# Kernel optimization log

Measured on AMD Instinct MI355X. Metric: run time of the kernel, lower is better.

Reference implementation:

```python
import jax, jax.numpy as jnp
import numpy as np

D = 1024
H = 16
HD = D // H
DS = 64
B, L = 2, 2048


def setup_inputs() -> dict:
    key = jax.random.key(0)
    ks = jax.random.split(key, 12)
    s = 0.02
    return {
        "x": jax.random.normal(ks[0], (B, L, D), jnp.float32),
        "subject_embed": jax.random.normal(ks[1], (B, DS), jnp.float32),
        "key_padding_mask": jnp.zeros((B, L), jnp.bool_),
        "Wq": jax.random.normal(ks[2], (D, D), jnp.float32) * s,
        "Wk": jax.random.normal(ks[3], (D, D), jnp.float32) * s,
        "Wv": jax.random.normal(ks[4], (D, D), jnp.float32) * s,
        "Wo": jax.random.normal(ks[5], (D, D), jnp.float32) * s,
        "bo": jnp.zeros((D,), jnp.float32),
        "Wsq": jax.random.normal(ks[6], (DS, D), jnp.float32) * s,
        "bsq": jnp.zeros((D,), jnp.float32),
        "Wsk": jax.random.normal(ks[7], (DS, D), jnp.float32) * s,
        "bsk": jnp.zeros((D,), jnp.float32),
    }


def reference(x, subject_embed, key_padding_mask, Wq, Wk, Wv, Wo, bo, Wsq, bsq, Wsk, bsk):
    scale = 1.0 / jnp.sqrt(jnp.asarray(HD, x.dtype))
    q = x @ Wq + (subject_embed @ Wsq + bsq)[:, None, :]   # [B,L,D]
    k = x @ Wk + (subject_embed @ Wsk + bsk)[:, None, :]
    v = x @ Wv
    # split heads: [B,H,L,hd]
    q = q.reshape(B, L, H, HD).transpose(0, 2, 1, 3)
    k = k.reshape(B, L, H, HD).transpose(0, 2, 1, 3)
    v = v.reshape(B, L, H, HD).transpose(0, 2, 1, 3)
    attn = jnp.einsum('bhqd,bhkd->bhqk', q, k) * scale      # [B,H,L,L]
    attn = jnp.where(key_padding_mask[:, None, None, :], -jnp.inf, attn)
    attn = jax.nn.softmax(attn, axis=-1)
    out = jnp.einsum('bhqk,bhkd->bhqd', attn, v)
    out = out.transpose(0, 2, 1, 3).reshape(B, L, D)
    return out @ Wo + bo
```

## Files before the change

### kernel.cpp

```cpp
#include <hip/hip_runtime.h>
#include <hip/hip_bf16.h>
#include <math.h>

#define DEV __device__ __forceinline__

typedef short bf16x8 __attribute__((ext_vector_type(8)));
typedef short bf16x4 __attribute__((ext_vector_type(4)));
typedef float f32x4 __attribute__((ext_vector_type(4)));

static constexpr int D  = 1024;
static constexpr int H  = 16;
static constexpr int HD = 64;
static constexpr int DS = 64;
static constexpr int B  = 2;
static constexpr int L  = 2048;
static constexpr int M  = B * L;

static constexpr float QSCALE = 0.18033688011112042f;

DEV unsigned short f2bf(float f) {
  union { float f; unsigned u; } x; x.f = f;
  unsigned r = (x.u + 0x7FFFu + ((x.u >> 16) & 1u)) >> 16;
  return (unsigned short)r;
}

DEV unsigned pack2bf(float a, float b) {
  return (unsigned)f2bf(a) | ((unsigned)f2bf(b) << 16);
}

DEV unsigned pack2bf_trunc(float a, float b) {
  union { float f; unsigned u; } ua{a}, ub{b};
  return (ua.u >> 16) | (ub.u & 0xffff0000u);
}

DEV void gload_lds16(const void* g, void* l) {
  __builtin_amdgcn_global_load_lds(
      (const __attribute__((address_space(1))) unsigned int*)g,
      (__attribute__((address_space(3))) unsigned int*)l, 16, 0, 0);
}

__global__ __launch_bounds__(256) void prep_kernel(
    const float* __restrict__ Wq, const float* __restrict__ Wk,
    const float* __restrict__ Wv, const float* __restrict__ Wo,
    const float* __restrict__ x, const float* __restrict__ subj,
    const float* __restrict__ Wsq, const float* __restrict__ bsq,
    const float* __restrict__ Wsk, const float* __restrict__ bsk,
    unsigned short* __restrict__ WT4, unsigned short* __restrict__ xb,
    float* __restrict__ sq, float* __restrict__ sk) {
  __shared__ float tile[64][65];
  const int blk = blockIdx.x, t = threadIdx.x;
  if (blk < 1024) {
    const int z = blk >> 8, idx = blk & 255;
    const float* W = z == 0 ? Wq : z == 1 ? Wk : z == 2 ? Wv : Wo;
    unsigned short* dst = WT4 + (size_t)z * D * D;
    const int n0 = (idx & 15) * 64, k0 = (idx >> 4) * 64;
    const int c = t & 63, r4 = t >> 6;
#pragma unroll
    for (int rr = 0; rr < 16; ++rr) {
      int row = r4 + rr * 4;
      tile[row][c] = W[(size_t)(k0 + row) * D + n0 + c];
    }
    __syncthreads();
#pragma unroll
    for (int rr = 0; rr < 16; ++rr) {
      int nrow = r4 + rr * 4;
      dst[(size_t)(n0 + nrow) * D + k0 + c] = f2bf(tile[c][nrow]);
    }
  } else if (blk < 3072) {
    size_t g = (size_t)(blk - 1024) * 256 + t;
    const float4* xf = (const float4*)x;
    float4 a = xf[2 * g], b = xf[2 * g + 1];
    union { unsigned short s[8]; uint4 v; } o;
    o.s[0] = f2bf(a.x); o.s[1] = f2bf(a.y); o.s[2] = f2bf(a.z); o.s[3] = f2bf(a.w);
    o.s[4] = f2bf(b.x); o.s[5] = f2bf(b.y); o.s[6] = f2bf(b.z); o.s[7] = f2bf(b.w);
    ((uint4*)xb)[g] = o.v;
  } else {
    int g = (blk - 3072) * 256 + t;
    int ty = g >> 11, b = (g >> 10) & 1, n = g & 1023;
    const float* W = ty ? Wsk : Wsq;
    const float* bias = ty ? bsk : bsq;
    float s = bias[n];
#pragma unroll 8
    for (int d = 0; d < DS; ++d) s += subj[b * DS + d] * W[d * D + n];
    (ty ? sk : sq)[b * D + n] = s;
  }
}

__global__ __launch_bounds__(256) void proj_kernel(
    const unsigned short* __restrict__ xb, const unsigned short* __restrict__ WT3,
    const float* __restrict__ sq, const float* __restrict__ sk,
    unsigned short* __restrict__ qk, unsigned short* __restrict__ vT) {
  __shared__ __align__(16) unsigned short smem[128 * 136];
  unsigned short* As = smem;
  unsigned short* Bs = smem + 128 * 64;
  const int z = blockIdx.z;
  const unsigned short* Wt = WT3 + (size_t)z * D * D;
  const int m0 = blockIdx.y * 128, n0 = blockIdx.x * 128;
  const int t = threadIdx.x, l = t & 63, w = t >> 6;
  const int wm = w >> 1, wn = w & 1;
  const int lm = l & 15, lq = l >> 4;
  const int srow8 = t >> 3;
  const int fsw = ((t & 7) ^ ((t >> 3) & 7)) * 8;
  const int swm = lm & 7;
  f32x4 acc[4][4] = {};
  for (int kt = 0; kt < D / 64; ++kt) {
    const int kb = kt * 64;
#pragma unroll
    for (int c = 0; c < 4; ++c) {
      int row = 32 * c + srow8;
      gload_lds16(&xb[(size_t)(m0 + row) * D + kb + fsw], &As[(32 * c + 8 * w) * 64]);
      gload_lds16(&Wt[(size_t)(n0 + row) * D + kb + fsw], &Bs[(32 * c + 8 * w) * 64]);
    }
    __syncthreads();
#pragma unroll
    for (int kk = 0; kk < 2; ++kk) {
      bf16x8 af[4], bf[4];
#pragma unroll
      for (int i = 0; i < 4; ++i)
        af[i] = *(const bf16x8*)&As[(64 * wm + 16 * i + lm) * 64 + ((kk * 4 + lq) ^ swm) * 8];
#pragma unroll
      for (int j = 0; j < 4; ++j)
        bf[j] = *(const bf16x8*)&Bs[(64 * wn + 16 * j + lm) * 64 + ((kk * 4 + lq) ^ swm) * 8];
#pragma unroll
      for (int i = 0; i < 4; ++i)
#pragma unroll
        for (int j = 0; j < 4; ++j)
          acc[i][j] = __builtin_amdgcn_mfma_f32_16x16x32_bf16(af[i], bf[j], acc[i][j], 0, 0, 0);
    }
    __syncthreads();
  }
  if (z == 2) {
#pragma unroll
    for (int i = 0; i < 4; ++i)
#pragma unroll
      for (int j = 0; j < 4; ++j) {
        int cr = 64 * wn + 16 * j + lm;
        int rr = 64 * wm + 16 * i + 4 * lq;
        uint2 u;
        u.x = pack2bf(acc[i][j][0], acc[i][j][1]);
        u.y = pack2bf(acc[i][j][2], acc[i][j][3]);
        *(uint2*)&smem[cr * 136 + rr] = u;
      }
    __syncthreads();
    const int cr = t >> 1, half = t & 1;
    const int bb = m0 >> 11, l0 = m0 & (L - 1);
    const int gcol = n0 + cr, h = gcol >> 6, hd = gcol & 63;
    size_t dbase = ((size_t)(bb * H + h) * HD + hd) * L + l0 + half * 64;
#pragma unroll
    for (int c = 0; c < 8; ++c) {
      uint4 u = *(const uint4*)&smem[cr * 136 + half * 64 + c * 8];
      *(uint4*)&vT[dbase + c * 8] = u;
    }
  } else {
    unsigned short* dst = qk + (size_t)z * M * D;
    const float* bias = z == 0 ? sq : sk;
    const float post = z == 0 ? QSCALE : 1.0f;
#pragma unroll
    for (int i = 0; i < 4; ++i)
#pragma unroll
      for (int j = 0; j < 4; ++j)
#pragma unroll
        for (int r = 0; r < 4; ++r) {
          int rr = 64 * wm + 16 * i + 4 * lq + r;
          int cc = 64 * wn + 16 * j + lm;
          float v = (acc[i][j][r] + bias[((m0 + rr) >> 11) * D + n0 + cc]) * post;
          smem[rr * 136 + cc] = f2bf(v);
        }
    __syncthreads();
    const int row = t >> 1, half = t & 1;
    const int bb = m0 >> 11, ll = (m0 & (L - 1)) + row;
    const int h0 = (n0 >> 6) + half;
    size_t dbase = ((size_t)(bb * H + h0) * L + ll) * HD;
#pragma unroll
    for (int c = 0; c < 8; ++c) {
      uint4 u = *(const uint4*)&smem[row * 136 + half * 64 + c * 8];
      *(uint4*)&dst[dbase + c * 8] = u;
    }
  }
}

__global__ __launch_bounds__(512, 4) void attn_kernel(
    const unsigned short* __restrict__ q_hm, const unsigned short* __restrict__ k_hm,
    const unsigned short* __restrict__ vT, const unsigned char* __restrict__ mask,
    unsigned short* __restrict__ ctx) {
  __shared__ __align__(16) unsigned short smem[40960];
  unsigned short* Qs  = smem;
  unsigned short* Ksb = smem + 8192;
  unsigned short* Vtb = smem + 24576;
  const int bx = blockIdx.x;
  const int rest = bx >> 3;
  const int bhid = (bx & 7) + 8 * (rest >> 4);
  const int q0 = (rest & 15) * 128;
  const int h = bhid & 15, b = bhid >> 4;
  const size_t bh = (size_t)(b * H + h);
  const unsigned short* qp = q_hm + bh * L * HD;
  const unsigned short* kp = k_hm + bh * L * HD;
  const unsigned short* vp = vT + bh * HD * L;
  const int t = threadIdx.x, l = t & 63, w = t >> 6;
  const int wq = w & 3, wj = w >> 2;
  const int lm = l & 15, lq = l >> 4;
  const int fsw = ((t & 7) ^ ((t >> 3) & 7)) * 8;
  const int swm = lm & 7;
  const int srow = t >> 3;
  const int vs = t & 15, vr = t >> 4;
  const int vcsrc = ((vs & 8) | ((vs & 7) ^ (vr & 7))) * 8;

#pragma unroll
  for (int c = 0; c < 2; ++c) {
    gload_lds16(&qp[(size_t)(q0 + 64 * c + srow) * HD + fsw], &Qs[(64 * c + 8 * w) * 64]);
    gload_lds16(&kp[(size_t)(64 * c + srow) * HD + fsw], &Ksb[(64 * c + 8 * w) * 64]);
    gload_lds16(&vp[(size_t)(32 * c + vr) * L + vcsrc], &Vtb[(32 * c + 4 * w) * 128]);
  }
  __syncthreads();
  bf16x8 qf[2][2];
#pragma unroll
  for (int i = 0; i < 2; ++i)
#pragma unroll
    for (int kk = 0; kk < 2; ++kk)
      qf[i][kk] = *(const bf16x8*)&Qs[(wq * 32 + 16 * i + lm) * 64 + ((kk * 4 + lq) ^ swm) * 8];

  float lsum[2] = {0.f, 0.f};
  f32x4 ot[2][4] = {};

  for (int kt = 0; kt < L / 128; ++kt) {
    const int cur = kt & 1;
    const unsigned short* Kc = Ksb + cur * 8192;
    const unsigned short* Vc = Vtb + cur * 8192;
    unsigned char mby = mask[b * L + kt * 128 + 64 * wj + l];
    if (kt + 1 < L / 128) {
      const int nk0 = (kt + 1) * 128;
      unsigned short* Kd = Ksb + (cur ^ 1) * 8192;
      unsigned short* Vd = Vtb + (cur ^ 1) * 8192;
#pragma unroll
      for (int c = 0; c < 2; ++c) {
        gload_lds16(&kp[(size_t)(nk0 + 64 * c + srow) * HD + fsw], &Kd[(64 * c + 8 * w) * 64]);
        gload_lds16(&vp[(size_t)(32 * c + vr) * L + nk0 + vcsrc], &Vd[(32 * c + 4 * w) * 128]);
      }
    }
    unsigned long long mb = __ballot(mby != 0);

#pragma unroll
    for (int jt4 = 0; jt4 < 4; ++jt4) {
      const int jt = 4 * wj + jt4;
      bf16x8 kf0 = *(const bf16x8*)&Kc[(16 * jt + lm) * 64 + ((0 + lq) ^ swm) * 8];
      bf16x8 kf1 = *(const bf16x8*)&Kc[(16 * jt + lm) * 64 + ((4 + lq) ^ swm) * 8];
      f32x4 st[2];
#pragma unroll
      for (int i = 0; i < 2; ++i) {
        f32x4 a = {};
        a = __builtin_amdgcn_mfma_f32_16x16x32_bf16(kf0, qf[i][0], a, 0, 0, 0);
        a = __builtin_amdgcn_mfma_f32_16x16x32_bf16(kf1, qf[i][1], a, 0, 0, 0);
        st[i] = a;
      }
      if (mb) {
        unsigned bits = (unsigned)(mb >> (4 * lq + 16 * jt4));
#pragma unroll
        for (int i = 0; i < 2; ++i)
#pragma unroll
          for (int r = 0; r < 4; ++r)
            if ((bits >> r) & 1u) st[i][r] = -1e30f;
      }
      union { uint2 u; bf16x4 v; } pp[2];
#pragma unroll
      for (int i = 0; i < 2; ++i) {
        f32x4 p;
        float ps = 0.f;
#pragma unroll
        for (int r = 0; r < 4; ++r) {
          float e = __builtin_amdgcn_exp2f(st[i][r]);
          p[r] = e;
          ps += e;
        }
        lsum[i] += ps;
        pp[i].u.x = pack2bf_trunc(p[0], p[1]);
        pp[i].u.y = pack2bf_trunc(p[2], p[3]);
      }
      const int kc2 = 2 * jt + (lq >> 1);
      const int slot = (kc2 & 8) | ((kc2 & 7) ^ swm);
#pragma unroll
      for (int jf = 0; jf < 4; ++jf) {
        bf16x4 vb = *(const bf16x4*)&Vc[(16 * jf + lm) * 128 + slot * 8 + 4 * (lq & 1)];
#pragma unroll
        for (int i = 0; i < 2; ++i)
          ot[i][jf] = __builtin_amdgcn_mfma_f32_16x16x16bf16_1k(
              pp[i].v, vb, ot[i][jf], 0, 0, 0);
      }
    }
    __syncthreads();
  }

  float* Obuf = (float*)smem;
  unsigned short* Es = smem + 20480;
  float* Sred = (float*)(smem + 35840);

  float sums[2];
#pragma unroll
  for (int i = 0; i < 2; ++i) {
    float s = lsum[i];
    s += __shfl_xor(s, 16, 64);
    s += __shfl_xor(s, 32, 64);
    sums[i] = s;
    Sred[w * 32 + i * 16 + lm] = s;
  }
  if (wj) {
#pragma unroll
    for (int i = 0; i < 2; ++i)
#pragma unroll
      for (int jf = 0; jf < 4; ++jf)
        *(f32x4*)&Obuf[(16 * jf + lm) * 132 + wq * 32 + 16 * i + 4 * lq] = ot[i][jf];
  }
  __syncthreads();
  if (!wj) {
    float rl[2];
#pragma unroll
    for (int i = 0; i < 2; ++i)
      rl[i] = 1.0f / (sums[i] + Sred[(w + 4) * 32 + i * 16 + lm]);
#pragma unroll
    for (int i = 0; i < 2; ++i)
#pragma unroll
      for (int jf = 0; jf < 4; ++jf) {
        f32x4 po = *(const f32x4*)&Obuf[(16 * jf + lm) * 132 + wq * 32 + 16 * i + 4 * lq];
        ot[i][jf] += po;
      }
#pragma unroll
    for (int i = 0; i < 2; ++i) {
      float rlq[4];
#pragma unroll
      for (int r = 0; r < 4; ++r) rlq[r] = __shfl(rl[i], 4 * lq + r, 64);
#pragma unroll
      for (int jf = 0; jf < 4; ++jf)
#pragma unroll
        for (int r = 0; r < 4; ++r)
          Es[(wq * 32 + 16 * i + 4 * lq + r) * 72 + 16 * jf + lm] =
              f2bf(ot[i][jf][r] * rlq[r]);
    }
    int row = l >> 1, half = l & 1;
    size_t obase = ((size_t)(b * L + q0 + wq * 32 + row)) * D + h * HD + half * 32;
#pragma unroll
    for (int c = 0; c < 4; ++c) {
      uint4 u = *(const uint4*)&Es[(wq * 32 + row) * 72 + half * 32 + c * 8];
      *(uint4*)&ctx[obase + c * 8] = u;
    }
  }
}

__global__ __launch_bounds__(256) void outgemm_kernel(
    const unsigned short* __restrict__ ctx, const unsigned short* __restrict__ WoT,
    const float* __restrict__ bo, float* __restrict__ out) {
  __shared__ unsigned short As[64 * 64];
  __shared__ unsigned short Bs[128 * 64];
  const int m0 = blockIdx.y * 64, n0 = blockIdx.x * 128;
  const int t = threadIdx.x, l = t & 63, w = t >> 6;
  const int wm = w >> 1, wn = w & 1;
  const int lm = l & 15, lq = l >> 4;
  const int srow8 = t >> 3;
  const int fsw = ((t & 7) ^ ((t >> 3) & 7)) * 8;
  const int swm = lm & 7;
  f32x4 acc[2][4] = {};
  for (int kt = 0; kt < D / 64; ++kt) {
    const int kb = kt * 64;
#pragma unroll
    for (int c = 0; c < 2; ++c)
      gload_lds16(&ctx[(size_t)(m0 + 32 * c + srow8) * D + kb + fsw],
                  &As[(32 * c + 8 * w) * 64]);
#pragma unroll
    for (int c = 0; c < 4; ++c)
      gload_lds16(&WoT[(size_t)(n0 + 32 * c + srow8) * D + kb + fsw],
                  &Bs[(32 * c + 8 * w) * 64]);
    __syncthreads();
#pragma unroll
    for (int kk = 0; kk < 2; ++kk) {
      bf16x8 af[2], bf[4];
#pragma unroll
      for (int i = 0; i < 2; ++i)
        af[i] = *(const bf16x8*)&As[(32 * wm + 16 * i + lm) * 64 + ((kk * 4 + lq) ^ swm) * 8];
#pragma unroll
      for (int j = 0; j < 4; ++j)
        bf[j] = *(const bf16x8*)&Bs[(64 * wn + 16 * j + lm) * 64 + ((kk * 4 + lq) ^ swm) * 8];
#pragma unroll
      for (int i = 0; i < 2; ++i)
#pragma unroll
        for (int j = 0; j < 4; ++j)
          acc[i][j] = __builtin_amdgcn_mfma_f32_16x16x32_bf16(af[i], bf[j], acc[i][j], 0, 0, 0);
    }
    __syncthreads();
  }
#pragma unroll
  for (int i = 0; i < 2; ++i)
#pragma unroll
    for (int j = 0; j < 4; ++j)
#pragma unroll
      for (int r = 0; r < 4; ++r) {
        int grow = m0 + 32 * wm + 16 * i + lq * 4 + r;
        int gcol = n0 + 64 * wn + 16 * j + lm;
        out[(size_t)grow * D + gcol] = acc[i][j][r] + bo[gcol];
      }
}

extern "C" void kernel_launch(void* const* d_in, const int* in_sizes, int n_in,
                              void* d_out, int out_size, void* d_ws, size_t ws_size,
                              hipStream_t stream) {
  const float* x    = (const float*)d_in[0];
  const float* subj = (const float*)d_in[1];
  const unsigned char* mask = (const unsigned char*)d_in[2];
  const float* Wq = (const float*)d_in[3];
  const float* Wk = (const float*)d_in[4];
  const float* Wv = (const float*)d_in[5];
  const float* Wo = (const float*)d_in[6];
  const float* bo = (const float*)d_in[7];
  const float* Wsq = (const float*)d_in[8];
  const float* bsq = (const float*)d_in[9];
  const float* Wsk = (const float*)d_in[10];
  const float* bsk = (const float*)d_in[11];
  float* out = (float*)d_out;
  char* ws = (char*)d_ws;

  unsigned short* xb  = (unsigned short*)(ws);
  unsigned short* WT4 = (unsigned short*)(ws + (8ull  << 20));
  unsigned short* qk  = (unsigned short*)(ws + (16ull << 20));
  unsigned short* ctx = (unsigned short*)(ws + (32ull << 20));
  unsigned short* vT  = (unsigned short*)(ws + (40ull << 20));
  float* sq = (float*)(ws + (48ull << 20));
  float* sk = sq + B * D;

  hipLaunchKernelGGL(prep_kernel, dim3(3088), dim3(256), 0, stream,
                     Wq, Wk, Wv, Wo, x, subj, Wsq, bsq, Wsk, bsk, WT4, xb, sq, sk);
  hipLaunchKernelGGL(proj_kernel, dim3(8, 32, 3), dim3(256), 0, stream,
                     xb, WT4, sq, sk, qk, vT);
  hipLaunchKernelGGL(attn_kernel, dim3(512), dim3(512), 0, stream,
                     qk, qk + (size_t)M * D, vT, mask, ctx);
  hipLaunchKernelGGL(outgemm_kernel, dim3(8, 64, 1), dim3(256), 0, stream, ctx,
                     WT4 + 3ull * D * D, bo, out);
}
```

Before: 207.1 us.

## Use 16x16x32 MFMA for PV by pairing key tiles with permuted K rows

Processes key tiles in pairs of 32 rows, choosing a permuted K-row mapping so each lane's QK^T outputs from two 16-key tiles can be packed into an 8-element bf16 operand. The PV product then uses the 16x16x32 bf16 MFMA with 16-byte V loads instead of twice as many 16x16x16 MFMAs with 8-byte loads. Mask bit extraction is adjusted to the new row permutation. This halves PV MFMA issue count and V LDS reads, at the cost of more live registers and lane-dependent select logic.

```diff
diff --git a/kernel.cpp b/kernel.cpp
--- a/kernel.cpp
+++ b/kernel.cpp
@@ -204,6 +204,10 @@
   const int srow = t >> 3;
   const int vs = t & 15, vr = t >> 4;
   const int vcsrc = ((vs & 8) | ((vs & 7) ^ (vr & 7))) * 8;
+  const int krow0 = 8 * (lm >> 2) + 4 * ((lm >> 2) & 1) + (lm & 3);
+  const int ks0 = krow0 & 7;
+  const int krow1 = krow0 ^ 4;
+  const int ks1 = ks0 ^ 4;
 
 #pragma unroll
   for (int c = 0; c < 2; ++c) {
@@ -240,50 +244,67 @@
     unsigned long long mb = __ballot(mby != 0);
 
 #pragma unroll
-    for (int jt4 = 0; jt4 < 4; ++jt4) {
-      const int jt = 4 * wj + jt4;
-      bf16x8 kf0 = *(const bf16x8*)&Kc[(16 * jt + lm) * 64 + ((0 + lq) ^ swm) * 8];
-      bf16x8 kf1 = *(const bf16x8*)&Kc[(16 * jt + lm) * 64 + ((4 + lq) ^ swm) * 8];
-      f32x4 st[2];
+    for (int g = 0; g < 2; ++g) {
+      const int gg = 2 * wj + g;
+      const unsigned short* Kg = Kc + 32 * gg * 64;
+      bf16x8 ka0 = *(const bf16x8*)&Kg[krow0 * 64 + ((0 + lq) ^ ks0) * 8];
+      bf16x8 ka1 = *(const bf16x8*)&Kg[krow0 * 64 + ((4 + lq) ^ ks0) * 8];
+      bf16x8 kb0 = *(const bf16x8*)&Kg[krow1 * 64 + ((0 + lq) ^ ks1) * 8];
+      bf16x8 kb1 = *(const bf16x8*)&Kg[krow1 * 64 + ((4 + lq) ^ ks1) * 8];
+      f32x4 stA[2], stB[2];
 #pragma unroll
       for (int i = 0; i < 2; ++i) {
         f32x4 a = {};
-        a = __builtin_amdgcn_mfma_f32_16x16x32_bf16(kf0, qf[i][0], a, 0, 0, 0);
-        a = __builtin_amdgcn_mfma_f32_16x16x32_bf16(kf1, qf[i][1], a, 0, 0, 0);
-        st[i] = a;
+        a = __builtin_amdgcn_mfma_f32_16x16x32_bf16(ka0, qf[i][0], a, 0, 0, 0);
+        a = __builtin_amdgcn_mfma_f32_16x16x32_bf16(ka1, qf[i][1], a, 0, 0, 0);
+        stA[i] = a;
+        f32x4 bq = {};
+        bq = __builtin_amdgcn_mfma_f32_16x16x32_bf16(kb0, qf[i][0], bq, 0, 0, 0);
+        bq = __builtin_amdgcn_mfma_f32_16x16x32_bf16(kb1, qf[i][1], bq, 0, 0, 0);
+        stB[i] = bq;
       }
       if (mb) {
-        unsigned bits = (unsigned)(mb >> (4 * lq + 16 * jt4));
+        const int shA = 32 * g + 8 * lq + 4 * (lq & 1);
+        unsigned bitsA = (unsigned)(mb >> shA);
+        unsigned bitsB = (unsigned)(mb >> (shA ^ 4));
 #pragma unroll
         for (int i = 0; i < 2; ++i)
 #pragma unroll
-          for (int r = 0; r < 4; ++r)
-            if ((bits >> r) & 1u) st[i][r] = -1e30f;
-      }
-      union { uint2 u; bf16x4 v; } pp[2];
+          for (int r = 0; r < 4; ++r) {
+            if ((bitsA >> r) & 1u) stA[i][r] = -1e30f;
+            if ((bitsB >> r) & 1u) stB[i][r] = -1e30f;
+          }
+      }
+      union { uint4 q; bf16x8 v; } pa[2];
+      const bool sw = (lq & 1) != 0;
 #pragma unroll
       for (int i = 0; i < 2; ++i) {
-        f32x4 p;
+        float eA[4], eB[4];
         float ps = 0.f;
 #pragma unroll
         for (int r = 0; r < 4; ++r) {
-          float e = __builtin_amdgcn_exp2f(st[i][r]);
-          p[r] = e;
-          ps += e;
+          eA[r] = __builtin_amdgcn_exp2f(stA[i][r]);
+          eB[r] = __builtin_amdgcn_exp2f(stB[i][r]);
+          ps += eA[r] + eB[r];
         }
         lsum[i] += ps;
-        pp[i].u.x = pack2bf_trunc(p[0], p[1]);
-        pp[i].u.y = pack2bf_trunc(p[2], p[3]);
-      }
-      const int kc2 = 2 * jt + (lq >> 1);
-      const int slot = (kc2 & 8) | ((kc2 & 7) ^ swm);
+        unsigned a01 = pack2bf_trunc(eA[0], eA[1]);
+        unsigned a23 = pack2bf_trunc(eA[2], eA[3]);
+        unsigned b01 = pack2bf_trunc(eB[0], eB[1]);
+        unsigned b23 = pack2bf_trunc(eB[2], eB[3]);
+        pa[i].q.x = sw ? b01 : a01;
+        pa[i].q.y = sw ? b23 : a23;
+        pa[i].q.z = sw ? a01 : b01;
+        pa[i].q.w = sw ? a23 : b23;
+      }
+      const int kc = 4 * gg + lq;
+      const int slot = (kc & 8) | ((kc & 7) ^ swm);
 #pragma unroll
       for (int jf = 0; jf < 4; ++jf) {
-        bf16x4 vb = *(const bf16x4*)&Vc[(16 * jf + lm) * 128 + slot * 8 + 4 * (lq & 1)];
+        bf16x8 vb = *(const bf16x8*)&Vc[(16 * jf + lm) * 128 + slot * 8];
 #pragma unroll
         for (int i = 0; i < 2; ++i)
-          ot[i][jf] = __builtin_amdgcn_mfma_f32_16x16x16bf16_1k(
-              pp[i].v, vb, ot[i][jf], 0, 0, 0);
+          ot[i][jf] = __builtin_amdgcn_mfma_f32_16x16x32_bf16(pa[i].v, vb, ot[i][jf], 0, 0, 0);
       }
     }
     __syncthreads();
```

New measurement: 204.7 us. About the same (-1.2%).
